# Optimization experiments

Measured on AMD Instinct MI355X. Metric: run time of the kernel, lower is better.

Reference implementation:

```python
import jax, jax.numpy as jnp
import numpy as np

D_MODEL = 512
DK = 4
DV = 8
HIDD = 10
HEAD = D_MODEL // DV  # 64
LN_EPS = 1e-5


def setup_inputs() -> dict:
    key = jax.random.key(0)
    ks = jax.random.split(key, 10)
    B, S, Se = 8, 512, 512
    u = jax.random.uniform  # torch.rand initializer for attention weights
    n = jax.random.normal
    return {
        "x": n(ks[0], (B, S, D_MODEL), jnp.float32),
        "x_enc": n(ks[1], (B, Se, D_MODEL), jnp.float32),
        "WqM": u(ks[2], (D_MODEL, HEAD * DK), jnp.float32),
        "WkM": u(ks[3], (D_MODEL, HEAD * DK), jnp.float32),
        "WvM": u(ks[4], (D_MODEL, HEAD * DV), jnp.float32),
        "ln_g": jnp.ones((D_MODEL,), jnp.float32),
        "ln_b": jnp.zeros((D_MODEL,), jnp.float32),
        "fc1_w": n(ks[5], (HIDD, D_MODEL), jnp.float32) * (1.0 / np.sqrt(D_MODEL)),
        "fc1_b": jnp.zeros((HIDD,), jnp.float32),
        "fc2_w": n(ks[6], (D_MODEL, HIDD), jnp.float32) * (1.0 / np.sqrt(HIDD)),
        "fc2_b": jnp.zeros((D_MODEL,), jnp.float32),
    }


def _attention(Xq, Xkv, WqM, WkM, WvM, causal_mul_mask):
    # NOTE: cross-attention in the source also uses WqM/WkM/WvM (Wq/Wk/Wv unused).
    B, Sq, _ = Xq.shape
    Sk = Xkv.shape[1]
    Q = (Xq @ WqM).reshape(B, Sq, HEAD, DK)
    K = (Xkv @ WkM).reshape(B, Sk, HEAD, DK)
    V = (Xkv @ WvM).reshape(B, Sk, HEAD, DV)
    score = jnp.einsum('bqhd,bkhd->bhqk', Q, K) / np.sqrt(DK).astype(np.float32)
    if causal_mul_mask:
        # Faithful quirk: multiplicative tril mask on scores (NOT additive -inf).
        score = score * jnp.tril(jnp.ones((Sq, Sk), score.dtype))
    w = jax.nn.softmax(score, axis=-1)
    out = jnp.einsum('bhqk,bkhd->bqhd', w, V)
    return out.reshape(B, Sq, HEAD * DV)  # HEAD*DV == d_model


def _layernorm(x, g, b):
    mu = jnp.mean(x, axis=-1, keepdims=True)
    var = jnp.mean(jnp.square(x - mu), axis=-1, keepdims=True)
    return (x - mu) * jax.lax.rsqrt(var + LN_EPS) * g + b


def reference(x, x_enc, WqM, WkM, WvM, ln_g, ln_b, fc1_w, fc1_b, fc2_w, fc2_b):
    fx = _attention(x, x, WqM, WkM, WvM, causal_mul_mask=True)
    fx = _attention(fx, x_enc, WqM, WkM, WvM, causal_mul_mask=False)
    y = _layernorm(x + fx, ln_g, ln_b)
    h = jax.nn.relu(y @ fc1_w.T + fc1_b)
    return h @ fc2_w.T + fc2_b
```

## Files before the change

### kernel.cpp

```cpp
#include <hip/hip_runtime.h>
#include <math.h>

#define D_MODEL 512
#define BATCH 8
#define SEQ 512
#define HEAD 64
#define DK 4
#define DV 8
#define HIDD 10

#define MR 32
#define KC 32
#define NC 128

__device__ __forceinline__ float4 fma4(float s, float4 w, float4 a) {
    a.x = fmaf(s, w.x, a.x); a.y = fmaf(s, w.y, a.y);
    a.z = fmaf(s, w.z, a.z); a.w = fmaf(s, w.w, a.w);
    return a;
}

__global__ __launch_bounds__(256, 8) void proj_kernel(
    const float* __restrict__ x, const float* __restrict__ xe,
    const float* __restrict__ Wq, const float* __restrict__ Wk,
    const float* __restrict__ Wv,
    float* __restrict__ Q1, float* __restrict__ K1, float* __restrict__ V1,
    float* __restrict__ Kc, float* __restrict__ Vc)
{
    __shared__ float xt[KC * MR];
    __shared__ float wt[KC * NC];

    const int t  = threadIdx.x;
    const int bj = blockIdx.x >> 7;
    const int br = blockIdx.x & 127;
    const int r0 = br * MR;

    const float* X; const float* W; int ldw; int c0; float* dst; int vtype;
    if (bj < 2)       { X = x;  W = Wq; ldw = 256; c0 = bj * 128;         dst = Q1; vtype = 0; }
    else if (bj < 4)  { X = x;  W = Wk; ldw = 256; c0 = (bj - 2) * 128;   dst = K1; vtype = 0; }
    else if (bj < 8)  { X = x;  W = Wv; ldw = 512; c0 = (bj - 4) * 128;   dst = V1; vtype = 1; }
    else if (bj < 10) { X = xe; W = Wk; ldw = 256; c0 = (bj - 8) * 128;   dst = Kc; vtype = 0; }
    else              { X = xe; W = Wv; ldw = 512; c0 = (bj - 10) * 128;  dst = Vc; vtype = 1; }

    const int cq = t & 31;
    const int rr = t >> 5;
    const int rs = t & 31;
    const int kq = t >> 5;

    float4 acc[4];
#pragma unroll
    for (int r = 0; r < 4; ++r) acc[r] = make_float4(0.f, 0.f, 0.f, 0.f);

    for (int kc = 0; kc < D_MODEL; kc += KC) {
        const float4 xa = *(const float4*)(X + (long)(r0 + rs) * D_MODEL + kc + kq * 4);
        xt[(kq * 4 + 0) * MR + rs] = xa.x;
        xt[(kq * 4 + 1) * MR + rs] = xa.y;
        xt[(kq * 4 + 2) * MR + rs] = xa.z;
        xt[(kq * 4 + 3) * MR + rs] = xa.w;

#pragma unroll
        for (int i = 0; i < 4; ++i) {
            const int row = i * 8 + (t >> 5);
            *(float4*)(wt + row * NC + (t & 31) * 4) =
                *(const float4*)(W + (long)(kc + row) * ldw + c0 + (t & 31) * 4);
        }
        __syncthreads();

#pragma unroll 4
        for (int k = 0; k < KC; ++k) {
            const float4 w4 = *(const float4*)(wt + k * NC + cq * 4);
            const float4 x4 = *(const float4*)(xt + k * MR + rr * 4);
            acc[0] = fma4(x4.x, w4, acc[0]);
            acc[1] = fma4(x4.y, w4, acc[1]);
            acc[2] = fma4(x4.z, w4, acc[2]);
            acc[3] = fma4(x4.w, w4, acc[3]);
        }
        __syncthreads();
    }

    const int b  = r0 >> 9;
    const int sb = (r0 & 511) + rr * 4;
    if (vtype == 0) {
        const int h = (c0 >> 2) + cq;
#pragma unroll
        for (int r = 0; r < 4; ++r)
            *(float4*)(dst + (((long)b * HEAD + h) * SEQ + sb + r) * 4) = acc[r];
    } else {
        const int col = c0 + cq * 4;
        const int h = col >> 3;
        const int off = col & 4;
#pragma unroll
        for (int r = 0; r < 4; ++r)
            *(float4*)(dst + (((long)b * HEAD + h) * SEQ + sb + r) * 8 + off) = acc[r];
    }
}

__global__ __launch_bounds__(256, 8) void proj2_kernel(
    const float* __restrict__ A, const float* __restrict__ Wq,
    float* __restrict__ Qa, float* __restrict__ Qb)
{
    __shared__ float xt[KC * MR];
    __shared__ float wt[KC * 64];

    const int t  = threadIdx.x;
    const int kh = blockIdx.x & 1;
    const int bj = (blockIdx.x >> 1) & 3;
    const int br = blockIdx.x >> 3;
    const int r0 = br * MR;
    const int c0 = bj * 64;
    const int kb = kh * 256;
    float* dst = kh ? Qb : Qa;

    const int cq = t & 15;
    const int rr = t >> 4;
    const int rs = t & 31, kq = t >> 5;

    float4 acc[2];
    acc[0] = make_float4(0.f, 0.f, 0.f, 0.f);
    acc[1] = acc[0];

    for (int kc = 0; kc < 256; kc += KC) {
        const float4 xa = *(const float4*)(A + (long)(r0 + rs) * D_MODEL + kb + kc + kq * 4);
        xt[(kq * 4 + 0) * MR + rs] = xa.x;
        xt[(kq * 4 + 1) * MR + rs] = xa.y;
        xt[(kq * 4 + 2) * MR + rs] = xa.z;
        xt[(kq * 4 + 3) * MR + rs] = xa.w;
#pragma unroll
        for (int i = 0; i < 2; ++i) {
            const int row = i * 16 + (t >> 4);
            *(float4*)(wt + row * 64 + (t & 15) * 4) =
                *(const float4*)(Wq + (long)(kb + kc + row) * 256 + c0 + (t & 15) * 4);
        }
        __syncthreads();
#pragma unroll 4
        for (int k = 0; k < KC; ++k) {
            const float4 w4 = *(const float4*)(wt + k * 64 + cq * 4);
            const float2 x2 = *(const float2*)(xt + k * MR + rr * 2);
            acc[0] = fma4(x2.x, w4, acc[0]);
            acc[1] = fma4(x2.y, w4, acc[1]);
        }
        __syncthreads();
    }

    const int b  = r0 >> 9;
    const int sb = (r0 & 511) + rr * 2;
    const int h  = (c0 >> 2) + cq;
#pragma unroll
    for (int r = 0; r < 2; ++r)
        *(float4*)(dst + (((long)b * HEAD + h) * SEQ + sb + r) * 4) = acc[r];
}

template <bool MASKED>
__device__ __forceinline__ void attn_scan(
    const float* __restrict__ Kl, const float* __restrict__ Vl, const int qb,
    const float q0, const float q1, const float q2, const float q3,
    float& m, float& l, float (&a)[8])
{
    for (int s0 = 0; s0 < 256; s0 += 8) {
        float sc[8];
#pragma unroll
        for (int i = 0; i < 8; ++i) {
            const float4 k4 = *(const float4*)(Kl + (s0 + i) * DK);
            const float d = fmaf(q0, k4.x, fmaf(q1, k4.y, fmaf(q2, k4.z, q3 * k4.w)));
            sc[i] = (MASKED && (s0 + i) > qb) ? 0.f : d;
        }
        const float gm = fmaxf(fmaxf(fmaxf(sc[0], sc[1]), fmaxf(sc[2], sc[3])),
                               fmaxf(fmaxf(sc[4], sc[5]), fmaxf(sc[6], sc[7])));
        if (gm > m) {
            const float scale = __builtin_amdgcn_exp2f(m - gm);
            l *= scale;
#pragma unroll
            for (int r = 0; r < 8; ++r) a[r] *= scale;
            m = gm;
        }
#pragma unroll
        for (int i = 0; i < 8; ++i) {
            const float p = __builtin_amdgcn_exp2f(sc[i] - m);
            l += p;
            const float4 v0 = *(const float4*)(Vl + (s0 + i) * DV);
            const float4 v1 = *(const float4*)(Vl + (s0 + i) * DV + 4);
            a[0] = fmaf(p, v0.x, a[0]); a[1] = fmaf(p, v0.y, a[1]);
            a[2] = fmaf(p, v0.z, a[2]); a[3] = fmaf(p, v0.w, a[3]);
            a[4] = fmaf(p, v1.x, a[4]); a[5] = fmaf(p, v1.y, a[5]);
            a[6] = fmaf(p, v1.z, a[6]); a[7] = fmaf(p, v1.w, a[7]);
        }
    }
}

__global__ __launch_bounds__(256, 8) void attn_kernel(
    const float* __restrict__ Qa, const float* __restrict__ Qb,
    const float* __restrict__ K2, const float* __restrict__ V2,
    float* __restrict__ PA, float* __restrict__ PM, const int causal)
{
    __shared__ float Kl[256 * DK];
    __shared__ float Vl[256 * DV];

    const int t  = threadIdx.x;
    const int bh = blockIdx.x >> 2;
    const int qh = (blockIdx.x >> 1) & 1;
    const int kh = blockIdx.x & 1;

    ((float4*)Kl)[t] = ((const float4*)(K2 + ((long)bh * SEQ + kh * 256) * DK))[t];
    const float4* Vs = (const float4*)(V2 + ((long)bh * SEQ + kh * 256) * DV);
    ((float4*)Vl)[t]       = Vs[t];
    ((float4*)Vl)[t + 256] = Vs[t + 256];

    const int q = qh * 256 + t;
    float4 qv = *(const float4*)(Qa + ((long)bh * SEQ + q) * DK);
    if (Qb) {
        const float4 qw = *(const float4*)(Qb + ((long)bh * SEQ + q) * DK);
        qv.x += qw.x; qv.y += qw.y; qv.z += qw.z; qv.w += qw.w;
    }
    const float cf = 0.5f * 1.44269504088896340736f;
    const float q0 = qv.x * cf, q1 = qv.y * cf, q2 = qv.z * cf, q3 = qv.w * cf;

    __syncthreads();

    float m = -INFINITY, l = 0.f, a[8];
#pragma unroll
    for (int r = 0; r < 8; ++r) a[r] = 0.f;

    if (causal)
        attn_scan<true >(Kl, Vl, q - kh * 256, q0, q1, q2, q3, m, l, a);
    else
        attn_scan<false>(Kl, Vl, 255,          q0, q1, q2, q3, m, l, a);

    const long p = ((long)(bh * 2 + kh)) * SEQ + q;
    *(float4*)(PA + p * 8)     = make_float4(a[0], a[1], a[2], a[3]);
    *(float4*)(PA + p * 8 + 4) = make_float4(a[4], a[5], a[6], a[7]);
    *(float2*)(PM + p * 2)     = make_float2(m, l);
}

__global__ __launch_bounds__(256) void combine_kernel(
    const float* __restrict__ PA, const float* __restrict__ PM,
    float* __restrict__ A)
{
    const int tid = blockIdx.x * 256 + threadIdx.x;
    const int bh  = tid >> 9;
    const int q   = tid & 511;
    const long p0 = ((long)bh * 2 + 0) * SEQ + q;
    const long p1 = ((long)bh * 2 + 1) * SEQ + q;
    const float2 ml0 = *(const float2*)(PM + p0 * 2);
    const float2 ml1 = *(const float2*)(PM + p1 * 2);
    const float M  = fmaxf(ml0.x, ml1.x);
    float w0 = __builtin_amdgcn_exp2f(ml0.x - M);
    float w1 = __builtin_amdgcn_exp2f(ml1.x - M);
    const float inv = 1.0f / fmaf(ml0.y, w0, ml1.y * w1);
    w0 *= inv; w1 *= inv;
    const float4 x0 = *(const float4*)(PA + p0 * 8);
    const float4 x1 = *(const float4*)(PA + p0 * 8 + 4);
    const float4 y0 = *(const float4*)(PA + p1 * 8);
    const float4 y1 = *(const float4*)(PA + p1 * 8 + 4);
    const int b = bh >> 6, h = bh & 63;
    float* dst = A + ((long)b * SEQ + q) * D_MODEL + h * DV;
    *(float4*)(dst)     = make_float4(x0.x*w0 + y0.x*w1, x0.y*w0 + y0.y*w1,
                                      x0.z*w0 + y0.z*w1, x0.w*w0 + y0.w*w1);
    *(float4*)(dst + 4) = make_float4(x1.x*w0 + y1.x*w1, x1.y*w0 + y1.y*w1,
                                      x1.z*w0 + y1.z*w1, x1.w*w0 + y1.w*w1);
}

__global__ __launch_bounds__(256) void ln_mlp_kernel(
    const float* __restrict__ x,
    const float* __restrict__ PA, const float* __restrict__ PM,
    const float* __restrict__ g, const float* __restrict__ beta,
    const float* __restrict__ w1, const float* __restrict__ b1,
    const float* __restrict__ w2, const float* __restrict__ b2,
    float* __restrict__ out)
{
    const int t = threadIdx.x;
    const int lane = t & 63;
    const int row = blockIdx.x * 4 + (t >> 6);
    const int b = row >> 9, q = row & 511;
    const long base = (long)row * D_MODEL;
    const int e0 = lane * 8;

    const long p0 = (((long)b * HEAD + lane) * 2 + 0) * SEQ + q;
    const long p1 = (((long)b * HEAD + lane) * 2 + 1) * SEQ + q;
    const float2 ml0 = *(const float2*)(PM + p0 * 2);
    const float2 ml1 = *(const float2*)(PM + p1 * 2);
    const float M  = fmaxf(ml0.x, ml1.x);
    float cw0 = __builtin_amdgcn_exp2f(ml0.x - M);
    float cw1 = __builtin_amdgcn_exp2f(ml1.x - M);
    const float inv = 1.0f / fmaf(ml0.y, cw0, ml1.y * cw1);
    cw0 *= inv; cw1 *= inv;
    const float4 fa0 = *(const float4*)(PA + p0 * 8);
    const float4 fa1 = *(const float4*)(PA + p0 * 8 + 4);
    const float4 fb0 = *(const float4*)(PA + p1 * 8);
    const float4 fb1 = *(const float4*)(PA + p1 * 8 + 4);

    const float4 xa = *(const float4*)(x + base + e0);
    const float4 xb = *(const float4*)(x + base + e0 + 4);
    float z[8] = {
        xa.x + fa0.x*cw0 + fb0.x*cw1, xa.y + fa0.y*cw0 + fb0.y*cw1,
        xa.z + fa0.z*cw0 + fb0.z*cw1, xa.w + fa0.w*cw0 + fb0.w*cw1,
        xb.x + fa1.x*cw0 + fb1.x*cw1, xb.y + fa1.y*cw0 + fb1.y*cw1,
        xb.z + fa1.z*cw0 + fb1.z*cw1, xb.w + fa1.w*cw0 + fb1.w*cw1};

    float sum = 0.f;
#pragma unroll
    for (int j = 0; j < 8; ++j) sum += z[j];
#pragma unroll
    for (int o = 32; o > 0; o >>= 1) sum += __shfl_xor(sum, o);
    const float mu = sum * (1.0f / 512.0f);

    float d[8], ss = 0.f;
#pragma unroll
    for (int j = 0; j < 8; ++j) { d[j] = z[j] - mu; ss += d[j] * d[j]; }
#pragma unroll
    for (int o = 32; o > 0; o >>= 1) ss += __shfl_xor(ss, o);
    const float rs = rsqrtf(ss * (1.0f / 512.0f) + 1e-5f);

    const float4 ga = *(const float4*)(g + e0);
    const float4 gb = *(const float4*)(g + e0 + 4);
    const float4 ba = *(const float4*)(beta + e0);
    const float4 bb = *(const float4*)(beta + e0 + 4);
    const float gg[8] = {ga.x,ga.y,ga.z,ga.w,gb.x,gb.y,gb.z,gb.w};
    const float bt[8] = {ba.x,ba.y,ba.z,ba.w,bb.x,bb.y,bb.z,bb.w};
    float y[8];
#pragma unroll
    for (int j = 0; j < 8; ++j) y[j] = d[j] * rs * gg[j] + bt[j];

    float part[HIDD];
#pragma unroll
    for (int i = 0; i < HIDD; ++i) {
        const float4 wa = *(const float4*)(w1 + i * 512 + e0);
        const float4 wb = *(const float4*)(w1 + i * 512 + e0 + 4);
        part[i] = y[0]*wa.x + y[1]*wa.y + y[2]*wa.z + y[3]*wa.w
                + y[4]*wb.x + y[5]*wb.y + y[6]*wb.z + y[7]*wb.w;
    }
#pragma unroll
    for (int i = 0; i < HIDD; ++i)
#pragma unroll
        for (int o = 32; o > 0; o >>= 1) part[i] += __shfl_xor(part[i], o);

    float hv[HIDD];
#pragma unroll
    for (int i = 0; i < HIDD; ++i) hv[i] = fmaxf(part[i] + b1[i], 0.f);

    const float4 b2a = *(const float4*)(b2 + e0);
    const float4 b2b = *(const float4*)(b2 + e0 + 4);
    float o8[8] = {b2a.x,b2a.y,b2a.z,b2a.w,b2b.x,b2b.y,b2b.z,b2b.w};
#pragma unroll
    for (int j = 0; j < 8; ++j) {
        const float* wr = w2 + (long)(e0 + j) * 10;
        const float2 wA = *(const float2*)(wr);
        const float2 wB = *(const float2*)(wr + 2);
        const float2 wC = *(const float2*)(wr + 4);
        const float2 wD = *(const float2*)(wr + 6);
        const float2 wE = *(const float2*)(wr + 8);
        o8[j] += hv[0]*wA.x + hv[1]*wA.y + hv[2]*wB.x + hv[3]*wB.y
               + hv[4]*wC.x + hv[5]*wC.y + hv[6]*wD.x + hv[7]*wD.y
               + hv[8]*wE.x + hv[9]*wE.y;
    }

    *(float4*)(out + base + e0)     = make_float4(o8[0], o8[1], o8[2], o8[3]);
    *(float4*)(out + base + e0 + 4) = make_float4(o8[4], o8[5], o8[6], o8[7]);
}

extern "C" void kernel_launch(void* const* d_in, const int* in_sizes, int n_in,
                              void* d_out, int out_size, void* d_ws, size_t ws_size,
                              hipStream_t stream) {
    (void)in_sizes; (void)n_in; (void)out_size; (void)ws_size;
    const float* x    = (const float*)d_in[0];
    const float* xenc = (const float*)d_in[1];
    const float* Wq   = (const float*)d_in[2];
    const float* Wk   = (const float*)d_in[3];
    const float* Wv   = (const float*)d_in[4];
    const float* ln_g = (const float*)d_in[5];
    const float* ln_b = (const float*)d_in[6];
    const float* w1   = (const float*)d_in[7];
    const float* b1   = (const float*)d_in[8];
    const float* w2   = (const float*)d_in[9];
    const float* b2   = (const float*)d_in[10];
    float* out = (float*)d_out;

    float* ws = (float*)d_ws;
    float* Q1 = ws;
    float* K1 = ws + 1048576;
    float* V1 = ws + 2097152;
    float* Kc = ws + 4194304;
    float* Vc = ws + 5242880;
    float* PA = ws + 7340032;
    float* PM = ws + 11534336;
    float* A  = K1;
    float* Qa = Q1;
    float* Qb = ws + 3145728;

    proj_kernel<<<dim3(1792), 256, 0, stream>>>(x, xenc, Wq, Wk, Wv,
                                                Q1, K1, V1, Kc, Vc);
    attn_kernel<<<dim3(2048), 256, 0, stream>>>(Q1, nullptr, K1, V1, PA, PM, 1);
    combine_kernel<<<dim3(1024), 256, 0, stream>>>(PA, PM, A);
    proj2_kernel<<<dim3(1024), 256, 0, stream>>>(A, Wq, Qa, Qb);
    attn_kernel<<<dim3(2048), 256, 0, stream>>>(Qa, Qb, Kc, Vc, PA, PM, 0);
    ln_mlp_kernel<<<dim3(1024), 256, 0, stream>>>(x, PA, PM, ln_g, ln_b,
                                                  w1, b1, w2, b2, out);
}
```

Baseline: 350.6 us.

## Enlarge projection row tile, shortcut fully-masked causal blocks, read K/V directly

The projection kernel now covers 64 rows per block with 8 float4 accumulators per thread, halving the grid and reusing each weight tile across more rows. In the causal attention pass, blocks whose keys all lie after their queries (kh=1, qh=0) have every score masked to zero, so their softmax is uniform. They now just sum V with wavefront shuffles and emit m=0, l=256 instead of running the exp/FMA scan, and the (kh=0, qh=1) blocks use the unmasked path. Attention also drops the shared-memory staging of K/V and reads them from global memory/cache directly. This trades extra register pressure in the projection kernel for reuse, and relies on cache for K/V reuse instead of LDS.

```diff
diff --git a/kernel.cpp b/kernel.cpp
--- a/kernel.cpp
+++ b/kernel.cpp
@@ -9,7 +9,7 @@
 #define DV 8
 #define HIDD 10
 
-#define MR 32
+#define MR 64
 #define KC 32
 #define NC 128
 
@@ -19,7 +19,7 @@
     return a;
 }
 
-__global__ __launch_bounds__(256, 8) void proj_kernel(
+__global__ __launch_bounds__(256, 4) void proj_kernel(
     const float* __restrict__ x, const float* __restrict__ xe,
     const float* __restrict__ Wq, const float* __restrict__ Wk,
     const float* __restrict__ Wv,
@@ -30,8 +30,8 @@
     __shared__ float wt[KC * NC];
 
     const int t  = threadIdx.x;
-    const int bj = blockIdx.x >> 7;
-    const int br = blockIdx.x & 127;
+    const int bj = blockIdx.x >> 6;
+    const int br = blockIdx.x & 63;
     const int r0 = br * MR;
 
     const float* X; const float* W; int ldw; int c0; float* dst; int vtype;
@@ -43,19 +43,25 @@
 
     const int cq = t & 31;
     const int rr = t >> 5;
-    const int rs = t & 31;
-    const int kq = t >> 5;
-
-    float4 acc[4];
-#pragma unroll
-    for (int r = 0; r < 4; ++r) acc[r] = make_float4(0.f, 0.f, 0.f, 0.f);
+    const int rs = t & 63;
+    const int kq = t >> 6;
+
+    float4 acc[8];
+#pragma unroll
+    for (int r = 0; r < 8; ++r) acc[r] = make_float4(0.f, 0.f, 0.f, 0.f);
 
     for (int kc = 0; kc < D_MODEL; kc += KC) {
-        const float4 xa = *(const float4*)(X + (long)(r0 + rs) * D_MODEL + kc + kq * 4);
+        const float* xrow = X + (long)(r0 + rs) * D_MODEL + kc;
+        const float4 xa = *(const float4*)(xrow + kq * 4);
+        const float4 xb = *(const float4*)(xrow + (kq + 4) * 4);
         xt[(kq * 4 + 0) * MR + rs] = xa.x;
         xt[(kq * 4 + 1) * MR + rs] = xa.y;
         xt[(kq * 4 + 2) * MR + rs] = xa.z;
         xt[(kq * 4 + 3) * MR + rs] = xa.w;
+        xt[((kq + 4) * 4 + 0) * MR + rs] = xb.x;
+        xt[((kq + 4) * 4 + 1) * MR + rs] = xb.y;
+        xt[((kq + 4) * 4 + 2) * MR + rs] = xb.z;
+        xt[((kq + 4) * 4 + 3) * MR + rs] = xb.w;
 
 #pragma unroll
         for (int i = 0; i < 4; ++i) {
@@ -68,28 +74,33 @@
 #pragma unroll 4
         for (int k = 0; k < KC; ++k) {
             const float4 w4 = *(const float4*)(wt + k * NC + cq * 4);
-            const float4 x4 = *(const float4*)(xt + k * MR + rr * 4);
-            acc[0] = fma4(x4.x, w4, acc[0]);
-            acc[1] = fma4(x4.y, w4, acc[1]);
-            acc[2] = fma4(x4.z, w4, acc[2]);
-            acc[3] = fma4(x4.w, w4, acc[3]);
+            const float4 x0 = *(const float4*)(xt + k * MR + rr * 8);
+            const float4 x1 = *(const float4*)(xt + k * MR + rr * 8 + 4);
+            acc[0] = fma4(x0.x, w4, acc[0]);
+            acc[1] = fma4(x0.y, w4, acc[1]);
+            acc[2] = fma4(x0.z, w4, acc[2]);
+            acc[3] = fma4(x0.w, w4, acc[3]);
+            acc[4] = fma4(x1.x, w4, acc[4]);
+            acc[5] = fma4(x1.y, w4, acc[5]);
+            acc[6] = fma4(x1.z, w4, acc[6]);
+            acc[7] = fma4(x1.w, w4, acc[7]);
         }
         __syncthreads();
     }
 
     const int b  = r0 >> 9;
-    const int sb = (r0 & 511) + rr * 4;
+    const int sb = (r0 & 511) + rr * 8;
     if (vtype == 0) {
         const int h = (c0 >> 2) + cq;
 #pragma unroll
-        for (int r = 0; r < 4; ++r)
+        for (int r = 0; r < 8; ++r)
             *(float4*)(dst + (((long)b * HEAD + h) * SEQ + sb + r) * 4) = acc[r];
     } else {
         const int col = c0 + cq * 4;
         const int h = col >> 3;
         const int off = col & 4;
 #pragma unroll
-        for (int r = 0; r < 4; ++r)
+        for (int r = 0; r < 8; ++r)
             *(float4*)(dst + (((long)b * HEAD + h) * SEQ + sb + r) * 8 + off) = acc[r];
     }
 }
@@ -98,14 +109,14 @@
     const float* __restrict__ A, const float* __restrict__ Wq,
     float* __restrict__ Qa, float* __restrict__ Qb)
 {
-    __shared__ float xt[KC * MR];
+    __shared__ float xt[KC * 32];
     __shared__ float wt[KC * 64];
 
     const int t  = threadIdx.x;
     const int kh = blockIdx.x & 1;
     const int bj = (blockIdx.x >> 1) & 3;
     const int br = blockIdx.x >> 3;
-    const int r0 = br * MR;
+    const int r0 = br * 32;
     const int c0 = bj * 64;
     const int kb = kh * 256;
     float* dst = kh ? Qb : Qa;
@@ -120,10 +131,10 @@
 
     for (int kc = 0; kc < 256; kc += KC) {
         const float4 xa = *(const float4*)(A + (long)(r0 + rs) * D_MODEL + kb + kc + kq * 4);
-        xt[(kq * 4 + 0) * MR + rs] = xa.x;
-        xt[(kq * 4 + 1) * MR + rs] = xa.y;
-        xt[(kq * 4 + 2) * MR + rs] = xa.z;
-        xt[(kq * 4 + 3) * MR + rs] = xa.w;
+        xt[(kq * 4 + 0) * 32 + rs] = xa.x;
+        xt[(kq * 4 + 1) * 32 + rs] = xa.y;
+        xt[(kq * 4 + 2) * 32 + rs] = xa.z;
+        xt[(kq * 4 + 3) * 32 + rs] = xa.w;
 #pragma unroll
         for (int i = 0; i < 2; ++i) {
             const int row = i * 16 + (t >> 4);
@@ -134,7 +145,7 @@
 #pragma unroll 4
         for (int k = 0; k < KC; ++k) {
             const float4 w4 = *(const float4*)(wt + k * 64 + cq * 4);
-            const float2 x2 = *(const float2*)(xt + k * MR + rr * 2);
+            const float2 x2 = *(const float2*)(xt + k * 32 + rr * 2);
             acc[0] = fma4(x2.x, w4, acc[0]);
             acc[1] = fma4(x2.y, w4, acc[1]);
         }
@@ -149,9 +160,9 @@
         *(float4*)(dst + (((long)b * HEAD + h) * SEQ + sb + r) * 4) = acc[r];
 }
 
-template <bool MASKED>
+template <int MASKED>
 __device__ __forceinline__ void attn_scan(
-    const float* __restrict__ Kl, const float* __restrict__ Vl, const int qb,
+    const float* __restrict__ Kp, const float* __restrict__ Vp, const int qb,
     const float q0, const float q1, const float q2, const float q3,
     float& m, float& l, float (&a)[8])
 {
@@ -159,7 +170,7 @@
         float sc[8];
 #pragma unroll
         for (int i = 0; i < 8; ++i) {
-            const float4 k4 = *(const float4*)(Kl + (s0 + i) * DK);
+            const float4 k4 = *(const float4*)(Kp + (s0 + i) * DK);
             const float d = fmaf(q0, k4.x, fmaf(q1, k4.y, fmaf(q2, k4.z, q3 * k4.w)));
             sc[i] = (MASKED && (s0 + i) > qb) ? 0.f : d;
         }
@@ -176,8 +187,8 @@
         for (int i = 0; i < 8; ++i) {
             const float p = __builtin_amdgcn_exp2f(sc[i] - m);
             l += p;
-            const float4 v0 = *(const float4*)(Vl + (s0 + i) * DV);
-            const float4 v1 = *(const float4*)(Vl + (s0 + i) * DV + 4);
+            const float4 v0 = *(const float4*)(Vp + (s0 + i) * DV);
+            const float4 v1 = *(const float4*)(Vp + (s0 + i) * DV + 4);
             a[0] = fmaf(p, v0.x, a[0]); a[1] = fmaf(p, v0.y, a[1]);
             a[2] = fmaf(p, v0.z, a[2]); a[3] = fmaf(p, v0.w, a[3]);
             a[4] = fmaf(p, v1.x, a[4]); a[5] = fmaf(p, v1.y, a[5]);
@@ -191,38 +202,53 @@
     const float* __restrict__ K2, const float* __restrict__ V2,
     float* __restrict__ PA, float* __restrict__ PM, const int causal)
 {
-    __shared__ float Kl[256 * DK];
-    __shared__ float Vl[256 * DV];
-
     const int t  = threadIdx.x;
     const int bh = blockIdx.x >> 2;
     const int qh = (blockIdx.x >> 1) & 1;
     const int kh = blockIdx.x & 1;
-
-    ((float4*)Kl)[t] = ((const float4*)(K2 + ((long)bh * SEQ + kh * 256) * DK))[t];
-    const float4* Vs = (const float4*)(V2 + ((long)bh * SEQ + kh * 256) * DV);
-    ((float4*)Vl)[t]       = Vs[t];
-    ((float4*)Vl)[t + 256] = Vs[t + 256];
-
-    const int q = qh * 256 + t;
-    float4 qv = *(const float4*)(Qa + ((long)bh * SEQ + q) * DK);
-    if (Qb) {
-        const float4 qw = *(const float4*)(Qb + ((long)bh * SEQ + q) * DK);
-        qv.x += qw.x; qv.y += qw.y; qv.z += qw.z; qv.w += qw.w;
-    }
-    const float cf = 0.5f * 1.44269504088896340736f;
-    const float q0 = qv.x * cf, q1 = qv.y * cf, q2 = qv.z * cf, q3 = qv.w * cf;
-
-    __syncthreads();
-
-    float m = -INFINITY, l = 0.f, a[8];
-#pragma unroll
-    for (int r = 0; r < 8; ++r) a[r] = 0.f;
-
-    if (causal)
-        attn_scan<true >(Kl, Vl, q - kh * 256, q0, q1, q2, q3, m, l, a);
-    else
-        attn_scan<false>(Kl, Vl, 255,          q0, q1, q2, q3, m, l, a);
+    const int q  = qh * 256 + t;
+
+    const float* Kp = K2 + ((long)bh * SEQ + kh * 256) * DK;
+    const float* Vp = V2 + ((long)bh * SEQ + kh * 256) * DV;
+
+    float m, l, a[8];
+
+    if (causal && kh == 1 && qh == 0) {
+        const int lane = t & 63;
+        float s[8] = {0.f,0.f,0.f,0.f,0.f,0.f,0.f,0.f};
+#pragma unroll
+        for (int i = 0; i < 4; ++i) {
+            const float4 v0 = *(const float4*)(Vp + (lane + i * 64) * DV);
+            const float4 v1 = *(const float4*)(Vp + (lane + i * 64) * DV + 4);
+            s[0]+=v0.x; s[1]+=v0.y; s[2]+=v0.z; s[3]+=v0.w;
+            s[4]+=v1.x; s[5]+=v1.y; s[6]+=v1.z; s[7]+=v1.w;
+        }
+#pragma unroll
+        for (int o = 32; o > 0; o >>= 1)
+#pragma unroll
+            for (int j = 0; j < 8; ++j) s[j] += __shfl_xor(s[j], o);
+        m = 0.f; l = 256.f;
+#pragma unroll
+        for (int j = 0; j < 8; ++j) a[j] = s[j];
+    } else {
+        float4 qv = *(const float4*)(Qa + ((long)bh * SEQ + q) * DK);
+        if (Qb) {
+            const float4 qw = *(const float4*)(Qb + ((long)bh * SEQ + q) * DK);
+            qv.x += qw.x; qv.y += qw.y; qv.z += qw.z; qv.w += qw.w;
+        }
+        const float cf = 0.5f * 1.44269504088896340736f;
+        const float q0 = qv.x * cf, q1 = qv.y * cf;
+        const float q2 = qv.z * cf, q3 = qv.w * cf;
+
+        m = -INFINITY; l = 0.f;
+#pragma unroll
+        for (int r = 0; r < 8; ++r) a[r] = 0.f;
+
+        if (!causal || (kh == 0 && qh == 1))
+            attn_scan<0>(Kp, Vp, 255, q0, q1, q2, q3, m, l, a);
+        else
+            attn_scan<1>(Kp, Vp, q - kh * 256, q0, q1, q2, q3, m, l, a);
+    }
 
     const long p = ((long)(bh * 2 + kh)) * SEQ + q;
     *(float4*)(PA + p * 8)     = make_float4(a[0], a[1], a[2], a[3]);
@@ -385,8 +411,8 @@
     float* Qa = Q1;
     float* Qb = ws + 3145728;
 
-    proj_kernel<<<dim3(1792), 256, 0, stream>>>(x, xenc, Wq, Wk, Wv,
-                                                Q1, K1, V1, Kc, Vc);
+    proj_kernel<<<dim3(896), 256, 0, stream>>>(x, xenc, Wq, Wk, Wv,
+                                               Q1, K1, V1, Kc, Vc);
     attn_kernel<<<dim3(2048), 256, 0, stream>>>(Q1, nullptr, K1, V1, PA, PM, 1);
     combine_kernel<<<dim3(1024), 256, 0, stream>>>(PA, PM, A);
     proj2_kernel<<<dim3(1024), 256, 0, stream>>>(A, Wq, Qa, Qb);
```

Result: slower. 364.5 us (+3.9%).
